# Performance work log

Measured on AMD Instinct MI355X. Metric: run time of the kernel, lower is better.

Reference implementation:

```python
import jax, jax.numpy as jnp
import numpy as np

N_EMBD = 1024
HEAD_SIZE = 64
B, T = 4, 4096


def setup_inputs() -> dict:
    key = jax.random.key(0)
    kx, kk, kq, kv = jax.random.split(key, 4)
    s = 1.0 / np.sqrt(N_EMBD)
    return {
        "x": jax.random.normal(kx, (B, T, N_EMBD), dtype=jnp.float32),
        "Wk": jax.random.normal(kk, (N_EMBD, HEAD_SIZE), dtype=jnp.float32) * s,
        "Wq": jax.random.normal(kq, (N_EMBD, HEAD_SIZE), dtype=jnp.float32) * s,
        "Wv": jax.random.normal(kv, (N_EMBD, HEAD_SIZE), dtype=jnp.float32) * s,
    }


def reference(x, Wk, Wq, Wv):
    Bb, Tt, C = x.shape
    k = x @ Wk  # [B,T,H]
    q = x @ Wq
    v = x @ Wv
    # scores scaled by C**-0.5 where C = n_embd (as in the original module)
    w = jnp.einsum('bth,bsh->bts', q, k) * (C ** -0.5)  # [B,T,T]
    causal = jnp.tril(jnp.ones((Tt, Tt), dtype=bool))
    w = jnp.where(causal, w, -jnp.inf)
    w = jax.nn.softmax(w, axis=-1)
    # dropout prob is 0.0 (eval) -> identity
    out = jnp.einsum('bts,bsh->bth', w, v)  # [B,T,H]
    return out
```

## Files before the change

### kernel.cpp

```cpp
#include <hip/hip_runtime.h>


#define BSZ 4
#define TSZ 4096
#define CSZ 1024
#define MSZ (BSZ * TSZ)
#define NS 8
#define QT 128
#define NQT (TSZ / QT)

typedef _Float16 half8 __attribute__((ext_vector_type(8)));
typedef _Float16 half4 __attribute__((ext_vector_type(4)));
typedef float f32x4 __attribute__((ext_vector_type(4)));

#define MFMA(a, b, c) __builtin_amdgcn_mfma_f32_16x16x32_f16((a), (b), (c), 0, 0, 0)
#define QSCALE 0.04508422002778011f

__device__ __forceinline__ int kimg(int r, int h) {
    return r * 64 + (((h >> 3) ^ (r & 7)) << 3) + (h & 7);
}
__device__ __forceinline__ int vimg(int kk, int h) {
    int p = (kk & 15) * 4 + (kk >> 4);
    return h * 64 + (((p >> 3) ^ (h & 7)) << 3) + (p & 7);
}

__device__ __forceinline__ void glds16(const _Float16* g, _Float16* l) {
    __builtin_amdgcn_global_load_lds(
        (const __attribute__((address_space(1))) void*)g,
        (__attribute__((address_space(3))) void*)l, 16, 0, 0);
}

__global__ __launch_bounds__(192) void wconv(const float* __restrict__ Wk,
                                             const float* __restrict__ Wq,
                                             const float* __restrict__ Wv,
                                             _Float16* __restrict__ Wt) {
    int k = blockIdx.x;
    int n = threadIdx.x;
    int g = k >> 6, c = (k >> 3) & 7, j = k & 7;
    const float* W = (n < 64) ? Wk : ((n < 128) ? Wq : Wv);
    float v = W[k * 64 + (n & 63)];
    if (n >= 64 && n < 128) v *= QSCALE;
    Wt[(size_t)n * 1024 + g * 64 + ((c ^ (n & 7)) << 3) + j] = (_Float16)v;
}

__global__ __launch_bounds__(256, 2) void qkv_proj(
    const float* __restrict__ x, const _Float16* __restrict__ Wt,
    _Float16* __restrict__ qbf, _Float16* __restrict__ kbs,
    _Float16* __restrict__ vts) {
    __shared__ _Float16 wt[2][192 * 64];
    __shared__ _Float16 xt[2][32 * 64];

    int tid = threadIdx.x;
    int wave = tid >> 6, lane = tid & 63;
    int quad = lane >> 4, l16 = lane & 15;
    int row0 = blockIdx.x * 32;

    f32x4 acc[6];
#pragma unroll
    for (int i = 0; i < 6; i++) acc[i] = (f32x4){0.f, 0.f, 0.f, 0.f};

    int sr = tid >> 3, sc = tid & 7;
    const float* xrow = x + (size_t)(row0 + sr) * CSZ + sc * 8;
    f32x4 p0 = *(const f32x4*)xrow;
    f32x4 p1 = *(const f32x4*)(xrow + 4);

#pragma unroll
    for (int i = 0; i < 6; i++) {
        int g = i * 256 + tid;
        glds16(Wt + ((size_t)(g >> 3)) * 1024 + 0 + (g & 7) * 8,
               &wt[0][(size_t)tid * 8 + i * 2048]);
    }

    int cur = 0;
    for (int kc = 0; kc < CSZ; kc += 64, cur ^= 1) {
        {
            _Float16 tmp[8] __attribute__((aligned(16)));
#pragma unroll
            for (int i = 0; i < 4; i++) {
                tmp[i] = (_Float16)p0[i];
                tmp[4 + i] = (_Float16)p1[i];
            }
            *(half8*)&xt[cur][sr * 64 + ((sc ^ (sr & 7)) << 3)] = *(half8*)tmp;
        }
        __syncthreads();

        if (kc + 64 < CSZ) {
#pragma unroll
            for (int i = 0; i < 6; i++) {
                int g = i * 256 + tid;
                glds16(Wt + ((size_t)(g >> 3)) * 1024 + (kc + 64) + (g & 7) * 8,
                       &wt[cur ^ 1][(size_t)tid * 8 + i * 2048]);
            }
            p0 = *(const f32x4*)(xrow + kc + 64);
            p1 = *(const f32x4*)(xrow + kc + 68);
        }

#pragma unroll
        for (int ss = 0; ss < 2; ss++) {
            half8 a0 = *(half8*)&xt[cur][l16 * 64 +
                                         (((ss * 4 + quad) ^ (l16 & 7)) << 3)];
            half8 a1 = *(half8*)&xt[cur][(16 + l16) * 64 +
                                         (((ss * 4 + quad) ^ (l16 & 7)) << 3)];
#pragma unroll
            for (int j = 0; j < 3; j++) {
                int ct = wave * 3 + j;
                half8 bb = *(half8*)&wt[cur][(ct * 16 + l16) * 64 +
                                             (((ss * 4 + quad) ^ (l16 & 7))
                                              << 3)];
                acc[j * 2 + 0] = MFMA(a0, bb, acc[j * 2 + 0]);
                acc[j * 2 + 1] = MFMA(a1, bb, acc[j * 2 + 1]);
            }
        }
    }

#pragma unroll
    for (int j = 0; j < 3; j++) {
        int ct = wave * 3 + j;
        int kind = ct >> 2;
        int col = (ct & 3) * 16 + l16;
#pragma unroll
        for (int m = 0; m < 2; m++) {
#pragma unroll
            for (int r = 0; r < 4; r++) {
                int row = row0 + m * 16 + quad * 4 + r;
                _Float16 val = (_Float16)acc[j * 2 + m][r];
                if (kind == 0) {
                    kbs[((size_t)(row >> 6)) * 4096 + kimg(row & 63, col)] = val;
                } else if (kind == 1) {
                    qbf[(size_t)row * 64 + col] = val;
                } else {
                    vts[((size_t)(row >> 6)) * 4096 + vimg(row & 63, col)] = val;
                }
            }
        }
    }
}

__global__ __launch_bounds__(256) void attn_partial(
    const _Float16* __restrict__ qbf, const _Float16* __restrict__ kbs,
    const _Float16* __restrict__ vts, _Float16* __restrict__ opart,
    float* __restrict__ ml) {
    __shared__ _Float16 kt[2][4096];
    __shared__ _Float16 vt[2][4096];
    __shared__ _Float16 pt[QT * 64];

    int tid = threadIdx.x;
    int wave = tid >> 6, lane = tid & 63;
    int quad = lane >> 4, l16 = lane & 15;
    int s = blockIdx.x & (NS - 1);
    int qt = (blockIdx.x >> 3) & (NQT - 1);
    int b = blockIdx.x >> 8;
    int nt = 2 * (qt + 1);
    int lo = s * nt / NS, hi = (s + 1) * nt / NS;
    int part = (b * NQT + qt) * NS + s;

    if (lo >= hi) {
        if (tid < QT) ml[part * QT + tid] = 0.f;
        return;
    }

    const _Float16* qb = qbf + (size_t)b * TSZ * 64;
    const _Float16* kbs_b = kbs + (size_t)b * 64 * 4096;
    const _Float16* vts_b = vts + (size_t)b * 64 * 4096;

    int qrow = qt * QT + wave * 32;
    half8 aq[2][2];
#pragma unroll
    for (int st = 0; st < 2; st++)
#pragma unroll
        for (int ss = 0; ss < 2; ss++)
            aq[st][ss] = *(const half8*)&qb[(size_t)(qrow + st * 16 + l16) * 64 +
                                            ss * 32 + quad * 8];

    f32x4 o[2][4];
    float l_acc[2][4];
#pragma unroll
    for (int st = 0; st < 2; st++)
#pragma unroll
        for (int ct = 0; ct < 4; ct++) {
            o[st][ct] = (f32x4){0.f, 0.f, 0.f, 0.f};
            l_acc[st][ct] = 0.f;
        }

    int soff = wave * 512 + lane * 8;

    {
        const _Float16* ks = kbs_b + (size_t)lo * 4096 + soff;
        const _Float16* vs = vts_b + (size_t)lo * 4096 + soff;
        glds16(ks, &kt[0][soff]);
        glds16(ks + 2048, &kt[0][2048 + soff]);
        glds16(vs, &vt[0][soff]);
        glds16(vs + 2048, &vt[0][2048 + soff]);
    }

    int cur = 0;
    for (int kti = lo; kti < hi; kti++, cur ^= 1) {
        __syncthreads();
        if (kti + 1 < hi) {
            const _Float16* ks = kbs_b + (size_t)(kti + 1) * 4096 + soff;
            const _Float16* vs = vts_b + (size_t)(kti + 1) * 4096 + soff;
            glds16(ks, &kt[cur ^ 1][soff]);
            glds16(ks + 2048, &kt[cur ^ 1][2048 + soff]);
            glds16(vs, &vt[cur ^ 1][soff]);
            glds16(vs + 2048, &vt[cur ^ 1][2048 + soff]);
        }

        f32x4 sacc[2][4];
#pragma unroll
        for (int st = 0; st < 2; st++)
#pragma unroll
            for (int ct = 0; ct < 4; ct++)
                sacc[st][ct] = (f32x4){0.f, 0.f, 0.f, 0.f};
#pragma unroll
        for (int ss = 0; ss < 2; ss++) {
#pragma unroll
            for (int ct = 0; ct < 4; ct++) {
                half8 bb = *(half8*)&kt[cur][(ct * 16 + l16) * 64 +
                                             (((ss * 4 + quad) ^ (l16 & 7))
                                              << 3)];
                sacc[0][ct] = MFMA(aq[0][ss], bb, sacc[0][ct]);
                sacc[1][ct] = MFMA(aq[1][ss], bb, sacc[1][ct]);
            }
        }

        bool diag = (kti >= 2 * qt);
#pragma unroll
        for (int st = 0; st < 2; st++) {
#pragma unroll
            for (int r = 0; r < 4; r++) {
                int lrow = wave * 32 + st * 16 + quad * 4 + r;
                float pv[4];
#pragma unroll
                for (int ct = 0; ct < 4; ct++) {
                    float e = exp2f(sacc[st][ct][r]);
                    if (diag) {
                        int key = kti * 64 + ct * 16 + l16;
                        if (key > qt * QT + lrow) e = 0.f;
                    }
                    pv[ct] = e;
                }
                l_acc[st][r] += pv[0] + pv[1] + pv[2] + pv[3];
                half4 hp;
#pragma unroll
                for (int ct = 0; ct < 4; ct++) hp[ct] = (_Float16)pv[ct];
                int chunk = (l16 >> 1) ^ (lrow & 7);
                *(half4*)&pt[lrow * 64 + chunk * 8 + (l16 & 1) * 4] = hp;
            }
        }

#pragma unroll
        for (int ss = 0; ss < 2; ss++) {
            half8 ap0 = *(half8*)&pt[(wave * 32 + l16) * 64 +
                                     (((ss * 4 + quad) ^ (l16 & 7)) << 3)];
            half8 ap1 = *(half8*)&pt[(wave * 32 + 16 + l16) * 64 +
                                     (((ss * 4 + quad) ^ (l16 & 7)) << 3)];
#pragma unroll
            for (int ct = 0; ct < 4; ct++) {
                half8 bv = *(half8*)&vt[cur][(ct * 16 + l16) * 64 +
                                             (((ss * 4 + quad) ^ (l16 & 7))
                                              << 3)];
                o[0][ct] = MFMA(ap0, bv, o[0][ct]);
                o[1][ct] = MFMA(ap1, bv, o[1][ct]);
            }
        }
    }

#pragma unroll
    for (int off = 1; off < 16; off <<= 1) {
#pragma unroll
        for (int st = 0; st < 2; st++)
#pragma unroll
            for (int r = 0; r < 4; r++)
                l_acc[st][r] += __shfl_xor(l_acc[st][r], off);
    }

    _Float16* op = opart + (size_t)part * (QT * 64);
#pragma unroll
    for (int st = 0; st < 2; st++) {
#pragma unroll
        for (int r = 0; r < 4; r++) {
            int lrow = wave * 32 + st * 16 + quad * 4 + r;
            float li = l_acc[st][r];
            float inv = li > 0.f ? 1.f / li : 0.f;
#pragma unroll
            for (int ct = 0; ct < 4; ct++)
                op[lrow * 64 + ct * 16 + l16] = (_Float16)(o[st][ct][r] * inv);
            if (l16 == 0) ml[part * QT + lrow] = li;
        }
    }
}

__global__ __launch_bounds__(256) void combine(
    const _Float16* __restrict__ opart, const float* __restrict__ ml,
    float* __restrict__ out) {
    int tid = threadIdx.x;
    int row = blockIdx.x * 32 + (tid >> 3);
    int seg = (tid & 7) * 8;
    int b = row >> 12;
    int qt = (row >> 7) & (NQT - 1);
    int prow = row & (QT - 1);
    int pbase = (b * NQT + qt) * NS;

    float acc[8];
#pragma unroll
    for (int i = 0; i < 8; i++) acc[i] = 0.f;
    float lsum = 0.f;
#pragma unroll
    for (int s = 0; s < NS; s++) {
        float l = ml[(pbase + s) * QT + prow];
        lsum += l;
        half8 h = *(const half8*)&opart[(size_t)(pbase + s) * (QT * 64) +
                                        prow * 64 + seg];
#pragma unroll
        for (int i = 0; i < 8; i++) acc[i] += l * (float)h[i];
    }
    float inv = 1.f / lsum;
    float* ob = out + (size_t)row * 64 + seg;
#pragma unroll
    for (int i = 0; i < 8; i++) ob[i] = acc[i] * inv;
}

extern "C" void kernel_launch(void* const* d_in, const int* in_sizes, int n_in,
                              void* d_out, int out_size, void* d_ws,
                              size_t ws_size, hipStream_t stream) {
    (void)in_sizes; (void)n_in; (void)out_size; (void)ws_size;
    const float* x = (const float*)d_in[0];
    const float* Wk = (const float*)d_in[1];
    const float* Wq = (const float*)d_in[2];
    const float* Wv = (const float*)d_in[3];

    _Float16* Wt = (_Float16*)d_ws;
    _Float16* qbf = Wt + 192 * 1024;
    _Float16* kbs = qbf + (size_t)MSZ * 64;
    _Float16* vts = kbs + (size_t)MSZ * 64;
    _Float16* opart = vts + (size_t)MSZ * 64;
    float* ml = (float*)(opart + (size_t)BSZ * NQT * NS * QT * 64);

    wconv<<<1024, 192, 0, stream>>>(Wk, Wq, Wv, Wt);
    qkv_proj<<<MSZ / 32, 256, 0, stream>>>(x, Wt, qbf, kbs, vts);
    attn_partial<<<BSZ * NQT * NS, 256, 0, stream>>>(qbf, kbs, vts, opart, ml);
    combine<<<MSZ / 32, 256, 0, stream>>>(opart, ml, (float*)d_out);
}
```

Before: 154.7 us.

## Split causal attention into fixed 4-tile chunks and interleave K/V storage

Replaces the fixed 8-way split per query tile with a variable number of blocks, each covering at most four key tiles, so every block does a similar amount of work and no block launches empty. The block index is mapped to a (query tile, chunk) pair with a short search loop, and the combine kernel now loops over a per-tile chunk count. K and V tiles are also interleaved into one buffer so each step's loads come from one contiguous region. In exchange there are more, shorter blocks with their own prologue and partial writes, and more partial outputs for combine to read on late query tiles.

```diff
diff --git a/kernel.cpp b/kernel.cpp
--- a/kernel.cpp
+++ b/kernel.cpp
@@ -5,9 +5,10 @@
 #define TSZ 4096
 #define CSZ 1024
 #define MSZ (BSZ * TSZ)
-#define NS 8
 #define QT 128
 #define NQT (TSZ / QT)
+#define CPB 272
+#define MAXC 16
 
 typedef _Float16 half8 __attribute__((ext_vector_type(8)));
 typedef _Float16 half4 __attribute__((ext_vector_type(4)));
@@ -45,8 +46,7 @@
 
 __global__ __launch_bounds__(256, 2) void qkv_proj(
     const float* __restrict__ x, const _Float16* __restrict__ Wt,
-    _Float16* __restrict__ qbf, _Float16* __restrict__ kbs,
-    _Float16* __restrict__ vts) {
+    _Float16* __restrict__ qbf, _Float16* __restrict__ kvs) {
     __shared__ _Float16 wt[2][192 * 64];
     __shared__ _Float16 xt[2][32 * 64];
 
@@ -67,7 +67,7 @@
 #pragma unroll
     for (int i = 0; i < 6; i++) {
         int g = i * 256 + tid;
-        glds16(Wt + ((size_t)(g >> 3)) * 1024 + 0 + (g & 7) * 8,
+        glds16(Wt + ((size_t)(g >> 3)) * 1024 + (g & 7) * 8,
                &wt[0][(size_t)tid * 8 + i * 2048]);
     }
 
@@ -125,11 +125,12 @@
                 int row = row0 + m * 16 + quad * 4 + r;
                 _Float16 val = (_Float16)acc[j * 2 + m][r];
                 if (kind == 0) {
-                    kbs[((size_t)(row >> 6)) * 4096 + kimg(row & 63, col)] = val;
+                    kvs[((size_t)(row >> 6)) * 8192 + kimg(row & 63, col)] = val;
                 } else if (kind == 1) {
                     qbf[(size_t)row * 64 + col] = val;
                 } else {
-                    vts[((size_t)(row >> 6)) * 4096 + vimg(row & 63, col)] = val;
+                    kvs[((size_t)(row >> 6)) * 8192 + 4096 +
+                        vimg(row & 63, col)] = val;
                 }
             }
         }
@@ -137,9 +138,8 @@
 }
 
 __global__ __launch_bounds__(256) void attn_partial(
-    const _Float16* __restrict__ qbf, const _Float16* __restrict__ kbs,
-    const _Float16* __restrict__ vts, _Float16* __restrict__ opart,
-    float* __restrict__ ml) {
+    const _Float16* __restrict__ qbf, const _Float16* __restrict__ kvs,
+    _Float16* __restrict__ opart, float* __restrict__ ml) {
     __shared__ _Float16 kt[2][4096];
     __shared__ _Float16 vt[2][4096];
     __shared__ _Float16 pt[QT * 64];
@@ -147,21 +147,20 @@
     int tid = threadIdx.x;
     int wave = tid >> 6, lane = tid & 63;
     int quad = lane >> 4, l16 = lane & 15;
-    int s = blockIdx.x & (NS - 1);
-    int qt = (blockIdx.x >> 3) & (NQT - 1);
-    int b = blockIdx.x >> 8;
+
+    int id = blockIdx.x;
+    int b = id / CPB;
+    int id2 = id - b * CPB;
+    int qt = 0;
+    while (qt < NQT - 1 && (((qt + 2) * (qt + 2)) >> 2) <= id2) qt++;
+    int chunk = id2 - (((qt + 1) * (qt + 1)) >> 2);
     int nt = 2 * (qt + 1);
-    int lo = s * nt / NS, hi = (s + 1) * nt / NS;
-    int part = (b * NQT + qt) * NS + s;
-
-    if (lo >= hi) {
-        if (tid < QT) ml[part * QT + tid] = 0.f;
-        return;
-    }
+    int lo = chunk * 4;
+    int hi = min(lo + 4, nt);
+    int part = (b * NQT + qt) * MAXC + chunk;
 
     const _Float16* qb = qbf + (size_t)b * TSZ * 64;
-    const _Float16* kbs_b = kbs + (size_t)b * 64 * 4096;
-    const _Float16* vts_b = vts + (size_t)b * 64 * 4096;
+    const _Float16* kvb = kvs + (size_t)b * 64 * 8192;
 
     int qrow = qt * QT + wave * 32;
     half8 aq[2][2];
@@ -185,24 +184,22 @@
     int soff = wave * 512 + lane * 8;
 
     {
-        const _Float16* ks = kbs_b + (size_t)lo * 4096 + soff;
-        const _Float16* vs = vts_b + (size_t)lo * 4096 + soff;
-        glds16(ks, &kt[0][soff]);
-        glds16(ks + 2048, &kt[0][2048 + soff]);
-        glds16(vs, &vt[0][soff]);
-        glds16(vs + 2048, &vt[0][2048 + soff]);
+        const _Float16* p0 = kvb + (size_t)lo * 8192 + soff;
+        glds16(p0, &kt[0][soff]);
+        glds16(p0 + 2048, &kt[0][2048 + soff]);
+        glds16(p0 + 4096, &vt[0][soff]);
+        glds16(p0 + 6144, &vt[0][2048 + soff]);
     }
 
     int cur = 0;
     for (int kti = lo; kti < hi; kti++, cur ^= 1) {
         __syncthreads();
         if (kti + 1 < hi) {
-            const _Float16* ks = kbs_b + (size_t)(kti + 1) * 4096 + soff;
-            const _Float16* vs = vts_b + (size_t)(kti + 1) * 4096 + soff;
-            glds16(ks, &kt[cur ^ 1][soff]);
-            glds16(ks + 2048, &kt[cur ^ 1][2048 + soff]);
-            glds16(vs, &vt[cur ^ 1][soff]);
-            glds16(vs + 2048, &vt[cur ^ 1][2048 + soff]);
+            const _Float16* p0 = kvb + (size_t)(kti + 1) * 8192 + soff;
+            glds16(p0, &kt[cur ^ 1][soff]);
+            glds16(p0 + 2048, &kt[cur ^ 1][2048 + soff]);
+            glds16(p0 + 4096, &vt[cur ^ 1][soff]);
+            glds16(p0 + 6144, &vt[cur ^ 1][2048 + soff]);
         }
 
         f32x4 sacc[2][4];
@@ -243,8 +240,8 @@
                 half4 hp;
 #pragma unroll
                 for (int ct = 0; ct < 4; ct++) hp[ct] = (_Float16)pv[ct];
-                int chunk = (l16 >> 1) ^ (lrow & 7);
-                *(half4*)&pt[lrow * 64 + chunk * 8 + (l16 & 1) * 4] = hp;
+                int chk = (l16 >> 1) ^ (lrow & 7);
+                *(half4*)&pt[lrow * 64 + chk * 8 + (l16 & 1) * 4] = hp;
             }
         }
 
@@ -299,14 +296,14 @@
     int b = row >> 12;
     int qt = (row >> 7) & (NQT - 1);
     int prow = row & (QT - 1);
-    int pbase = (b * NQT + qt) * NS;
+    int pbase = (b * NQT + qt) * MAXC;
+    int nc = (qt + 2) >> 1;
 
     float acc[8];
 #pragma unroll
     for (int i = 0; i < 8; i++) acc[i] = 0.f;
     float lsum = 0.f;
-#pragma unroll
-    for (int s = 0; s < NS; s++) {
+    for (int s = 0; s < nc; s++) {
         float l = ml[(pbase + s) * QT + prow];
         lsum += l;
         half8 h = *(const half8*)&opart[(size_t)(pbase + s) * (QT * 64) +
@@ -331,13 +328,12 @@
 
     _Float16* Wt = (_Float16*)d_ws;
     _Float16* qbf = Wt + 192 * 1024;
-    _Float16* kbs = qbf + (size_t)MSZ * 64;
-    _Float16* vts = kbs + (size_t)MSZ * 64;
-    _Float16* opart = vts + (size_t)MSZ * 64;
-    float* ml = (float*)(opart + (size_t)BSZ * NQT * NS * QT * 64);
+    _Float16* kvs = qbf + (size_t)MSZ * 64;
+    _Float16* opart = kvs + (size_t)MSZ * 128;
+    float* ml = (float*)(opart + (size_t)BSZ * NQT * MAXC * QT * 64);
 
     wconv<<<1024, 192, 0, stream>>>(Wk, Wq, Wv, Wt);
-    qkv_proj<<<MSZ / 32, 256, 0, stream>>>(x, Wt, qbf, kbs, vts);
-    attn_partial<<<BSZ * NQT * NS, 256, 0, stream>>>(qbf, kbs, vts, opart, ml);
+    qkv_proj<<<MSZ / 32, 256, 0, stream>>>(x, Wt, qbf, kvs);
+    attn_partial<<<BSZ * CPB, 256, 0, stream>>>(qbf, kvs, opart, ml);
     combine<<<MSZ / 32, 256, 0, stream>>>(opart, ml, (float*)d_out);
 }
```

Result: no change. 152.0 us (-1.8%).
